# Performance work log

Hardware: AMD Instinct MI355X
Metric: run time of the kernel (lower is better)

## Reference

```python
import jax, jax.numpy as jnp
import numpy as np


def setup_inputs() -> dict:
    key = jax.random.key(0)
    k1, k2, k3, k4 = jax.random.split(key, 4)
    L, d, n_tokens = 4096, 2048, 4096
    x = jax.random.normal(k1, (L, d), dtype=jnp.float32)
    Wq_w = jax.random.normal(k2, (d, d), dtype=jnp.float32) * (1.0 / np.sqrt(d))
    Pk = jax.random.normal(k3, (1, n_tokens, d), dtype=jnp.float32)
    Pv = jax.random.normal(k4, (1, n_tokens, d), dtype=jnp.float32)
    return {"x": x, "Wq_w": Wq_w, "Pk": Pk, "Pv": Pv, "sliding_window_size": 1024}


def reference(x, Wq_w, Pk, Pv, sliding_window_size):
    # x: (L, d); Pk/Pv: (1, n_tokens, d). Single-head cross attention to a
    # fixed parameter token bank with a bidirectional sliding-window mask
    # |q_idx - kv_idx| < sliding_window_size (flex_attention semantics,
    # default scale = 1/sqrt(d)).
    L, d = x.shape
    n_tokens = Pk.shape[1]
    scale = 1.0 / np.sqrt(d).astype(np.float32)

    q = x @ Wq_w.T                                    # (L, d)
    scores = jnp.einsum('ld,td->lt', q, Pk[0]) * scale  # (L, n_tokens)

    q_idx = jnp.arange(L)[:, None]
    kv_idx = jnp.arange(n_tokens)[None, :]
    mask = jnp.abs(q_idx - kv_idx) < sliding_window_size  # (L, n_tokens)

    neg_inf = jnp.asarray(jnp.finfo(scores.dtype).min, scores.dtype)
    probs = jax.nn.softmax(jnp.where(mask, scores, neg_inf), axis=-1)
    y = jnp.einsum('lt,td->ld', probs, Pv[0])         # (L, d)
    return y[None, :, :]                              # (1, L, d) after squeeze(1)
```

## Files before the change

### kernel.cpp

```cpp
#include <hip/hip_runtime.h>


using bf16x8 = __attribute__((ext_vector_type(8))) short;
using f32x4  = __attribute__((ext_vector_type(4))) float;

#define LDIM 4096
#define TDIM 4096
#define DDIM 2048

static __device__ __forceinline__ unsigned short f2bf(float f) {
  union { float f; unsigned u; } c; c.f = f;
  unsigned r = c.u + 0x7FFFu + ((c.u >> 16) & 1u);
  return (unsigned short)(r >> 16);
}
static __device__ __forceinline__ unsigned pack2(float a, float b) {
  return (unsigned)f2bf(a) | ((unsigned)f2bf(b) << 16);
}
static __device__ __forceinline__ void gload16(const void* g, void* l) {
  __builtin_amdgcn_global_load_lds((const __attribute__((address_space(1))) void*)g,
                                   (__attribute__((address_space(3))) void*)l, 16, 0, 0);
}

__global__ __launch_bounds__(256) void k_prep(const float* __restrict__ x,
                                              const float* __restrict__ Wq,
                                              unsigned short* __restrict__ xb,
                                              unsigned short* __restrict__ wb) {
  const int tid = threadIdx.x;
  const int b = blockIdx.x;
  const float* in; unsigned short* out; size_t i;
  if (b < 4096) { in = x;  out = xb; i = (size_t)b * 256 + tid; }
  else          { in = Wq; out = wb; i = (size_t)(b - 4096) * 256 + tid; }
  const float4* p = (const float4*)(in + i * 8);
  float4 a = p[0], c = p[1];
  uint4 o = { pack2(a.x, a.y), pack2(a.z, a.w), pack2(c.x, c.y), pack2(c.z, c.w) };
  *(uint4*)(out + i * 8) = o;
}

static __device__ __forceinline__ void gemm_loop8(const unsigned short* __restrict__ A,
                                                  const unsigned short* __restrict__ B,
                                                  int m0, int n0, long lda, long ldb,
                                                  int kbeg, int kend,
                                                  unsigned short* As, unsigned short* Bs,
                                                  f32x4 (&acc)[4][2]) {
  const int tid = threadIdx.x;
  const int wave = tid >> 6, lane = tid & 63;
  const int quad = lane >> 4, l16 = lane & 15;
  const int wm = wave >> 2, wn = wave & 3;
  const int srow = wave * 16 + (lane >> 3);
  const int scb  = (lane & 7) ^ (lane >> 3);

  const unsigned short* gA = A + (long)(m0 + srow) * lda + scb * 8;
  const unsigned short* gB = B + (long)(n0 + srow) * ldb + scb * 8;
  unsigned short* lA = As + wave * 1024;
  unsigned short* lB = Bs + wave * 1024;

  const int sw = (l16 & 7) * 8;

  for (int k0 = kbeg; k0 < kend; k0 += 64) {
    gload16(gA + k0,           lA);
    gload16(gA + k0 + 8 * lda, lA + 512);
    gload16(gB + k0,           lB);
    gload16(gB + k0 + 8 * ldb, lB + 512);
    __syncthreads();
    bf16x8 af[4][2], bfr[2][2];
#pragma unroll
    for (int i = 0; i < 4; i++)
#pragma unroll
      for (int h = 0; h < 2; h++)
        af[i][h] = *(const bf16x8*)&As[(wm * 64 + i * 16 + l16) * 64 +
                                       (((h * 4 + quad) * 8) ^ sw)];
#pragma unroll
    for (int j = 0; j < 2; j++)
#pragma unroll
      for (int h = 0; h < 2; h++)
        bfr[j][h] = *(const bf16x8*)&Bs[(wn * 32 + j * 16 + l16) * 64 +
                                        (((h * 4 + quad) * 8) ^ sw)];
#pragma unroll
    for (int h = 0; h < 2; h++)
#pragma unroll
      for (int i = 0; i < 4; i++)
#pragma unroll
        for (int j = 0; j < 2; j++)
          acc[i][j] = __builtin_amdgcn_mfma_f32_16x16x32_bf16(af[i][h], bfr[j][h],
                                                              acc[i][j], 0, 0, 0);
    __syncthreads();
  }
}

__global__ __launch_bounds__(512) void k1_fused(const unsigned short* __restrict__ X,
                                                const unsigned short* __restrict__ W,
                                                const float* __restrict__ Pk,
                                                const float* __restrict__ Pv,
                                                unsigned short* __restrict__ q,
                                                unsigned short* __restrict__ kb,
                                                unsigned short* __restrict__ vt,
                                                float* __restrict__ rowsum) {
  __shared__ __align__(16) unsigned short As[128 * 64];
  __shared__ __align__(16) unsigned short Bs[128 * 64];
  const int tid = threadIdx.x;
  const int b = blockIdx.x;

  if (b < 512) {
    f32x4 acc[4][2] = {};
    const int m0 = (b >> 4) * 128, n0 = (b & 15) * 128;
    gemm_loop8(X, W, m0, n0, DDIM, DDIM, 0, DDIM, As, Bs, acc);
    const int wave = tid >> 6, lane = tid & 63;
    const int quad = lane >> 4, l16 = lane & 15, wm = wave >> 2, wn = wave & 3;
#pragma unroll
    for (int i = 0; i < 4; i++)
#pragma unroll
      for (int j = 0; j < 2; j++)
#pragma unroll
        for (int r = 0; r < 4; r++) {
          int row = m0 + wm * 64 + i * 16 + quad * 4 + r;
          int col = n0 + wn * 32 + j * 16 + l16;
          q[(long)row * DDIM + col] = f2bf(acc[i][j][r]);
        }
    return;
  }
  if (b < 2560) {
    size_t i = (size_t)(b - 512) * 512 + tid;
    const float4* p = (const float4*)(Pk + i * 8);
    float4 a = p[0], c = p[1];
    uint4 o = { pack2(a.x, a.y), pack2(a.z, a.w), pack2(c.x, c.y), pack2(c.z, c.w) };
    *(uint4*)(kb + i * 8) = o;
    return;
  }
  if (b == 4608) {
    for (int k = tid; k < LDIM; k += 512) rowsum[k] = 0.f;
    return;
  }
  unsigned short (*tile)[72] = (unsigned short (*)[72])As;
  const int b2 = b - 2560;
  const int t0 = (b2 & 63) * 64, j0 = (b2 >> 6) * 64;
  const int r = tid >> 4, c4 = (tid & 15) * 4;
#pragma unroll
  for (int rr = 0; rr < 64; rr += 32) {
    float4 v = *(const float4*)(Pv + (size_t)(t0 + r + rr) * DDIM + j0 + c4);
    tile[c4 + 0][r + rr] = f2bf(v.x);
    tile[c4 + 1][r + rr] = f2bf(v.y);
    tile[c4 + 2][r + rr] = f2bf(v.z);
    tile[c4 + 3][r + rr] = f2bf(v.w);
  }
  __syncthreads();
  const int jr = tid >> 3, tc = (tid & 7) * 8;
  *(uint4*)(vt + (size_t)(j0 + jr) * TDIM + t0 + tc) = *(const uint4*)&tile[jr][tc];
}

__global__ __launch_bounds__(512) void k2_qk(const unsigned short* __restrict__ Q,
                                             const unsigned short* __restrict__ Kb,
                                             unsigned short* __restrict__ P,
                                             float* __restrict__ rowsum,
                                             const int* __restrict__ wptr) {
  const int w = *wptr;
  const int l0 = blockIdx.y * 128, t0 = blockIdx.x * 128;
  int lo = l0 - w + 1; if (lo < 0) lo = 0;
  int hi = l0 + 127 + w - 1; if (hi > TDIM - 1) hi = TDIM - 1;
  if ((int)blockIdx.x < (lo >> 7) || (int)blockIdx.x > (hi >> 7)) return;
  __shared__ __align__(16) unsigned short As[128 * 64];
  __shared__ __align__(16) unsigned short Bs[128 * 64];
  f32x4 acc[4][2] = {};
  gemm_loop8(Q, Kb, l0, t0, DDIM, DDIM, 0, DDIM, As, Bs, acc);
  const float scale = 0.022097086912079608f;
  const int tid = threadIdx.x;
  const int wave = tid >> 6, lane = tid & 63;
  const int quad = lane >> 4, l16 = lane & 15, wm = wave >> 2, wn = wave & 3;
#pragma unroll
  for (int i = 0; i < 4; i++) {
    float rs[4] = {0.f, 0.f, 0.f, 0.f};
#pragma unroll
    for (int j = 0; j < 2; j++)
#pragma unroll
      for (int r = 0; r < 4; r++) {
        int l = l0 + wm * 64 + i * 16 + quad * 4 + r;
        int t = t0 + wn * 32 + j * 16 + l16;
        int dlt = l - t; dlt = dlt < 0 ? -dlt : dlt;
        float e = 0.f;
        if (dlt < w) e = __expf(acc[i][j][r] * scale);
        unsigned short bv = f2bf(e);
        P[(long)l * TDIM + t] = bv;
        rs[r] += __uint_as_float((unsigned)bv << 16);
      }
#pragma unroll
    for (int r = 0; r < 4; ++r) {
      float s = rs[r];
      s += __shfl_xor(s, 1);
      s += __shfl_xor(s, 2);
      s += __shfl_xor(s, 4);
      s += __shfl_xor(s, 8);
      if (l16 == 0) atomicAdd(&rowsum[l0 + wm * 64 + i * 16 + quad * 4 + r], s);
    }
  }
}

__global__ __launch_bounds__(512) void k3_pv(const unsigned short* __restrict__ P,
                                             const unsigned short* __restrict__ Vt,
                                             const float* __restrict__ rowsum,
                                             float* __restrict__ Y,
                                             const int* __restrict__ wptr) {
  const int w = *wptr;
  const int l0 = blockIdx.y * 128, j0 = blockIdx.x * 128;
  int lo = l0 - w + 1; if (lo < 0) lo = 0;
  int hi = l0 + 127 + w - 1; if (hi > TDIM - 1) hi = TDIM - 1;
  const int kb = (lo >> 7) * 128, ke = ((hi >> 7) + 1) * 128;
  __shared__ __align__(16) unsigned short As[128 * 64];
  __shared__ __align__(16) unsigned short Bs[128 * 64];
  f32x4 acc[4][2] = {};
  gemm_loop8(P, Vt, l0, j0, TDIM, TDIM, kb, ke, As, Bs, acc);
  const int tid = threadIdx.x;
  const int wave = tid >> 6, lane = tid & 63;
  const int quad = lane >> 4, l16 = lane & 15, wm = wave >> 2, wn = wave & 3;
#pragma unroll
  for (int i = 0; i < 4; i++)
#pragma unroll
    for (int r = 0; r < 4; r++) {
      const int l = l0 + wm * 64 + i * 16 + quad * 4 + r;
      const float inv = 1.0f / rowsum[l];
#pragma unroll
      for (int j = 0; j < 2; j++)
        Y[(long)l * DDIM + j0 + wn * 32 + j * 16 + l16] = acc[i][j][r] * inv;
    }
}

extern "C" void kernel_launch(void* const* d_in, const int* in_sizes, int n_in,
                              void* d_out, int out_size, void* d_ws, size_t ws_size,
                              hipStream_t stream) {
  const float* x  = (const float*)d_in[0];
  const float* Wq = (const float*)d_in[1];
  const float* Pk = (const float*)d_in[2];
  const float* Pv = (const float*)d_in[3];
  const int* wptr = (const int*)d_in[4];
  float* Y = (float*)d_out;

  unsigned short* base = (unsigned short*)d_ws;
  unsigned short* Pm = base;
  unsigned short* xb = base;
  unsigned short* wb = base + (size_t)LDIM * DDIM;
  unsigned short* kb = base + (size_t)TDIM * TDIM;
  unsigned short* vt = kb + (size_t)TDIM * DDIM;
  unsigned short* qb = vt + (size_t)DDIM * TDIM;
  float* rowsum = (float*)(qb + (size_t)LDIM * DDIM);

  k_prep<<<6144, 256, 0, stream>>>(x, Wq, xb, wb);
  k1_fused<<<4609, 512, 0, stream>>>(xb, wb, Pk, Pv, qb, kb, vt, rowsum);
  k2_qk<<<dim3(TDIM / 128, LDIM / 128), 512, 0, stream>>>(qb, kb, Pm, rowsum, wptr);
  k3_pv<<<dim3(DDIM / 128, LDIM / 128), 512, 0, stream>>>(Pm, vt, rowsum, Y, wptr);
}
```

Before: 270.7 us.

## Switch GEMMs to 1024-thread blocks with 128-wide K steps and 32x32 wave tiles

Rewrites the shared bf16 GEMM loop so each 128x128 block uses 16 waves instead of 8. Each wave computes a 32x32 sub-tile and the loop stages a 128-element K slice per iteration with a 16-way XOR swizzle. The aim is fewer barriers per K and more waves to hide latency. The cost is that each block needs twice the LDS (64KB) and each wave does fewer MFMAs per LDS fragment load. The prep/transpose branches of k1 are remapped to the new thread count, and the launch bounds now request 8 waves per EU, which may constrain register allocation.

Result: slower. 293.8 us (+8.5%).

```diff
diff --git a/kernel.cpp b/kernel.cpp
--- a/kernel.cpp
+++ b/kernel.cpp
@@ -36,143 +36,141 @@
   *(uint4*)(out + i * 8) = o;
 }
 
-static __device__ __forceinline__ void gemm_loop8(const unsigned short* __restrict__ A,
-                                                  const unsigned short* __restrict__ B,
-                                                  int m0, int n0, long lda, long ldb,
-                                                  int kbeg, int kend,
-                                                  unsigned short* As, unsigned short* Bs,
-                                                  f32x4 (&acc)[4][2]) {
+static __device__ __forceinline__ void gemm_loop16(const unsigned short* __restrict__ A,
+                                                   const unsigned short* __restrict__ B,
+                                                   int m0, int n0, long lda, long ldb,
+                                                   int kbeg, int kend,
+                                                   unsigned short* As, unsigned short* Bs,
+                                                   f32x4 (&acc)[2][2]) {
   const int tid = threadIdx.x;
   const int wave = tid >> 6, lane = tid & 63;
   const int quad = lane >> 4, l16 = lane & 15;
   const int wm = wave >> 2, wn = wave & 3;
-  const int srow = wave * 16 + (lane >> 3);
-  const int scb  = (lane & 7) ^ (lane >> 3);
-
-  const unsigned short* gA = A + (long)(m0 + srow) * lda + scb * 8;
-  const unsigned short* gB = B + (long)(n0 + srow) * ldb + scb * 8;
+  const int r0 = wave * 8 + (lane >> 4);
+  const int r1 = r0 + 4;
+  const int c  = lane & 15;
+  const int sc0 = c ^ (r0 & 15), sc1 = c ^ (r1 & 15);
+
+  const unsigned short* gA0 = A + (long)(m0 + r0) * lda + sc0 * 8;
+  const unsigned short* gA1 = A + (long)(m0 + r1) * lda + sc1 * 8;
+  const unsigned short* gB0 = B + (long)(n0 + r0) * ldb + sc0 * 8;
+  const unsigned short* gB1 = B + (long)(n0 + r1) * ldb + sc1 * 8;
   unsigned short* lA = As + wave * 1024;
   unsigned short* lB = Bs + wave * 1024;
 
-  const int sw = (l16 & 7) * 8;
-
-  for (int k0 = kbeg; k0 < kend; k0 += 64) {
-    gload16(gA + k0,           lA);
-    gload16(gA + k0 + 8 * lda, lA + 512);
-    gload16(gB + k0,           lB);
-    gload16(gB + k0 + 8 * ldb, lB + 512);
+  for (int k0 = kbeg; k0 < kend; k0 += 128) {
+    gload16(gA0 + k0, lA);
+    gload16(gA1 + k0, lA + 512);
+    gload16(gB0 + k0, lB);
+    gload16(gB1 + k0, lB + 512);
     __syncthreads();
-    bf16x8 af[4][2], bfr[2][2];
-#pragma unroll
-    for (int i = 0; i < 4; i++)
-#pragma unroll
-      for (int h = 0; h < 2; h++)
-        af[i][h] = *(const bf16x8*)&As[(wm * 64 + i * 16 + l16) * 64 +
-                                       (((h * 4 + quad) * 8) ^ sw)];
-#pragma unroll
-    for (int j = 0; j < 2; j++)
-#pragma unroll
-      for (int h = 0; h < 2; h++)
-        bfr[j][h] = *(const bf16x8*)&Bs[(wn * 32 + j * 16 + l16) * 64 +
-                                        (((h * 4 + quad) * 8) ^ sw)];
-#pragma unroll
-    for (int h = 0; h < 2; h++)
-#pragma unroll
-      for (int i = 0; i < 4; i++)
+#pragma unroll
+    for (int h = 0; h < 4; h++) {
+      bf16x8 af[2], bfr[2];
+#pragma unroll
+      for (int i = 0; i < 2; i++)
+        af[i] = *(const bf16x8*)&As[(wm * 32 + i * 16 + l16) * 128 +
+                                    (((h * 4 + quad) ^ l16) * 8)];
+#pragma unroll
+      for (int j = 0; j < 2; j++)
+        bfr[j] = *(const bf16x8*)&Bs[(wn * 32 + j * 16 + l16) * 128 +
+                                     (((h * 4 + quad) ^ l16) * 8)];
+#pragma unroll
+      for (int i = 0; i < 2; i++)
 #pragma unroll
         for (int j = 0; j < 2; j++)
-          acc[i][j] = __builtin_amdgcn_mfma_f32_16x16x32_bf16(af[i][h], bfr[j][h],
+          acc[i][j] = __builtin_amdgcn_mfma_f32_16x16x32_bf16(af[i], bfr[j],
                                                               acc[i][j], 0, 0, 0);
+    }
     __syncthreads();
   }
 }
 
-__global__ __launch_bounds__(512) void k1_fused(const unsigned short* __restrict__ X,
-                                                const unsigned short* __restrict__ W,
-                                                const float* __restrict__ Pk,
-                                                const float* __restrict__ Pv,
-                                                unsigned short* __restrict__ q,
-                                                unsigned short* __restrict__ kb,
-                                                unsigned short* __restrict__ vt,
-                                                float* __restrict__ rowsum) {
-  __shared__ __align__(16) unsigned short As[128 * 64];
-  __shared__ __align__(16) unsigned short Bs[128 * 64];
+__global__ __launch_bounds__(1024, 8) void k1_fused(const unsigned short* __restrict__ X,
+                                                    const unsigned short* __restrict__ W,
+                                                    const float* __restrict__ Pk,
+                                                    const float* __restrict__ Pv,
+                                                    unsigned short* __restrict__ q,
+                                                    unsigned short* __restrict__ kb,
+                                                    unsigned short* __restrict__ vt,
+                                                    float* __restrict__ rowsum) {
+  __shared__ __align__(16) unsigned short As[128 * 128];
+  __shared__ __align__(16) unsigned short Bs[128 * 128];
   const int tid = threadIdx.x;
   const int b = blockIdx.x;
 
   if (b < 512) {
-    f32x4 acc[4][2] = {};
+    f32x4 acc[2][2] = {};
     const int m0 = (b >> 4) * 128, n0 = (b & 15) * 128;
-    gemm_loop8(X, W, m0, n0, DDIM, DDIM, 0, DDIM, As, Bs, acc);
+    gemm_loop16(X, W, m0, n0, DDIM, DDIM, 0, DDIM, As, Bs, acc);
     const int wave = tid >> 6, lane = tid & 63;
     const int quad = lane >> 4, l16 = lane & 15, wm = wave >> 2, wn = wave & 3;
 #pragma unroll
-    for (int i = 0; i < 4; i++)
+    for (int i = 0; i < 2; i++)
 #pragma unroll
       for (int j = 0; j < 2; j++)
 #pragma unroll
         for (int r = 0; r < 4; r++) {
-          int row = m0 + wm * 64 + i * 16 + quad * 4 + r;
+          int row = m0 + wm * 32 + i * 16 + quad * 4 + r;
           int col = n0 + wn * 32 + j * 16 + l16;
           q[(long)row * DDIM + col] = f2bf(acc[i][j][r]);
         }
     return;
   }
-  if (b < 2560) {
-    size_t i = (size_t)(b - 512) * 512 + tid;
+  if (b < 1536) {
+    size_t i = (size_t)(b - 512) * 1024 + tid;
     const float4* p = (const float4*)(Pk + i * 8);
     float4 a = p[0], c = p[1];
     uint4 o = { pack2(a.x, a.y), pack2(a.z, a.w), pack2(c.x, c.y), pack2(c.z, c.w) };
     *(uint4*)(kb + i * 8) = o;
     return;
   }
-  if (b == 4608) {
-    for (int k = tid; k < LDIM; k += 512) rowsum[k] = 0.f;
+  if (b == 3584) {
+    for (int k = tid; k < LDIM; k += 1024) rowsum[k] = 0.f;
     return;
   }
   unsigned short (*tile)[72] = (unsigned short (*)[72])As;
-  const int b2 = b - 2560;
+  const int b2 = b - 1536;
   const int t0 = (b2 & 63) * 64, j0 = (b2 >> 6) * 64;
   const int r = tid >> 4, c4 = (tid & 15) * 4;
-#pragma unroll
-  for (int rr = 0; rr < 64; rr += 32) {
-    float4 v = *(const float4*)(Pv + (size_t)(t0 + r + rr) * DDIM + j0 + c4);
-    tile[c4 + 0][r + rr] = f2bf(v.x);
-    tile[c4 + 1][r + rr] = f2bf(v.y);
-    tile[c4 + 2][r + rr] = f2bf(v.z);
-    tile[c4 + 3][r + rr] = f2bf(v.w);
+  {
+    float4 v = *(const float4*)(Pv + (size_t)(t0 + r) * DDIM + j0 + c4);
+    tile[c4 + 0][r] = f2bf(v.x);
+    tile[c4 + 1][r] = f2bf(v.y);
+    tile[c4 + 2][r] = f2bf(v.z);
+    tile[c4 + 3][r] = f2bf(v.w);
   }
   __syncthreads();
-  const int jr = tid >> 3, tc = (tid & 7) * 8;
-  *(uint4*)(vt + (size_t)(j0 + jr) * TDIM + t0 + tc) = *(const uint4*)&tile[jr][tc];
-}
-
-__global__ __launch_bounds__(512) void k2_qk(const unsigned short* __restrict__ Q,
-                                             const unsigned short* __restrict__ Kb,
-                                             unsigned short* __restrict__ P,
-                                             float* __restrict__ rowsum,
-                                             const int* __restrict__ wptr) {
+  const int jr = tid >> 4, tc = (tid & 15) * 4;
+  *(uint2*)(vt + (size_t)(j0 + jr) * TDIM + t0 + tc) = *(const uint2*)&tile[jr][tc];
+}
+
+__global__ __launch_bounds__(1024, 8) void k2_qk(const unsigned short* __restrict__ Q,
+                                                 const unsigned short* __restrict__ Kb,
+                                                 unsigned short* __restrict__ P,
+                                                 float* __restrict__ rowsum,
+                                                 const int* __restrict__ wptr) {
   const int w = *wptr;
   const int l0 = blockIdx.y * 128, t0 = blockIdx.x * 128;
   int lo = l0 - w + 1; if (lo < 0) lo = 0;
   int hi = l0 + 127 + w - 1; if (hi > TDIM - 1) hi = TDIM - 1;
   if ((int)blockIdx.x < (lo >> 7) || (int)blockIdx.x > (hi >> 7)) return;
-  __shared__ __align__(16) unsigned short As[128 * 64];
-  __shared__ __align__(16) unsigned short Bs[128 * 64];
-  f32x4 acc[4][2] = {};
-  gemm_loop8(Q, Kb, l0, t0, DDIM, DDIM, 0, DDIM, As, Bs, acc);
+  __shared__ __align__(16) unsigned short As[128 * 128];
+  __shared__ __align__(16) unsigned short Bs[128 * 128];
+  f32x4 acc[2][2] = {};
+  gemm_loop16(Q, Kb, l0, t0, DDIM, DDIM, 0, DDIM, As, Bs, acc);
   const float scale = 0.022097086912079608f;
   const int tid = threadIdx.x;
   const int wave = tid >> 6, lane = tid & 63;
   const int quad = lane >> 4, l16 = lane & 15, wm = wave >> 2, wn = wave & 3;
 #pragma unroll
-  for (int i = 0; i < 4; i++) {
+  for (int i = 0; i < 2; i++) {
     float rs[4] = {0.f, 0.f, 0.f, 0.f};
 #pragma unroll
     for (int j = 0; j < 2; j++)
 #pragma unroll
       for (int r = 0; r < 4; r++) {
-        int l = l0 + wm * 64 + i * 16 + quad * 4 + r;
+        int l = l0 + wm * 32 + i * 16 + quad * 4 + r;
         int t = t0 + wn * 32 + j * 16 + l16;
         int dlt = l - t; dlt = dlt < 0 ? -dlt : dlt;
         float e = 0.f;
@@ -188,33 +186,33 @@
       s += __shfl_xor(s, 2);
       s += __shfl_xor(s, 4);
       s += __shfl_xor(s, 8);
-      if (l16 == 0) atomicAdd(&rowsum[l0 + wm * 64 + i * 16 + quad * 4 + r], s);
+      if (l16 == 0) atomicAdd(&rowsum[l0 + wm * 32 + i * 16 + quad * 4 + r], s);
     }
   }
 }
 
-__global__ __launch_bounds__(512) void k3_pv(const unsigned short* __restrict__ P,
-                                             const unsigned short* __restrict__ Vt,
-                                             const float* __restrict__ rowsum,
-                                             float* __restrict__ Y,
-                                             const int* __restrict__ wptr) {
+__global__ __launch_bounds__(1024, 8) void k3_pv(const unsigned short* __restrict__ P,
+                                                 const unsigned short* __restrict__ Vt,
+                                                 const float* __restrict__ rowsum,
+                                                 float* __restrict__ Y,
+                                                 const int* __restrict__ wptr) {
   const int w = *wptr;
   const int l0 = blockIdx.y * 128, j0 = blockIdx.x * 128;
   int lo = l0 - w + 1; if (lo < 0) lo = 0;
   int hi = l0 + 127 + w - 1; if (hi > TDIM - 1) hi = TDIM - 1;
   const int kb = (lo >> 7) * 128, ke = ((hi >> 7) + 1) * 128;
-  __shared__ __align__(16) unsigned short As[128 * 64];
-  __shared__ __align__(16) unsigned short Bs[128 * 64];
-  f32x4 acc[4][2] = {};
-  gemm_loop8(P, Vt, l0, j0, TDIM, TDIM, kb, ke, As, Bs, acc);
+  __shared__ __align__(16) unsigned short As[128 * 128];
+  __shared__ __align__(16) unsigned short Bs[128 * 128];
+  f32x4 acc[2][2] = {};
+  gemm_loop16(P, Vt, l0, j0, TDIM, TDIM, kb, ke, As, Bs, acc);
   const int tid = threadIdx.x;
   const int wave = tid >> 6, lane = tid & 63;
   const int quad = lane >> 4, l16 = lane & 15, wm = wave >> 2, wn = wave & 3;
 #pragma unroll
-  for (int i = 0; i < 4; i++)
+  for (int i = 0; i < 2; i++)
 #pragma unroll
     for (int r = 0; r < 4; r++) {
-      const int l = l0 + wm * 64 + i * 16 + quad * 4 + r;
+      const int l = l0 + wm * 32 + i * 16 + quad * 4 + r;
       const float inv = 1.0f / rowsum[l];
 #pragma unroll
       for (int j = 0; j < 2; j++)
@@ -242,7 +240,7 @@
   float* rowsum = (float*)(qb + (size_t)LDIM * DDIM);
 
   k_prep<<<6144, 256, 0, stream>>>(x, Wq, xb, wb);
-  k1_fused<<<4609, 512, 0, stream>>>(xb, wb, Pk, Pv, qb, kb, vt, rowsum);
-  k2_qk<<<dim3(TDIM / 128, LDIM / 128), 512, 0, stream>>>(qb, kb, Pm, rowsum, wptr);
-  k3_pv<<<dim3(DDIM / 128, LDIM / 128), 512, 0, stream>>>(Pm, vt, rowsum, Y, wptr);
-}
+  k1_fused<<<3585, 1024, 0, stream>>>(xb, wb, Pk, Pv, qb, kb, vt, rowsum);
+  k2_qk<<<dim3(TDIM / 128, LDIM / 128), 1024, 0, stream>>>(qb, kb, Pm, rowsum, wptr);
+  k3_pv<<<dim3(DDIM / 128, LDIM / 128), 1024, 0, stream>>>(Pm, vt, rowsum, Y, wptr);
+}
```

## Merge all stages into one persistent cooperative kernel with grid syncs

Applied to the files above, without the earlier changes.

Replaces the four separate launches (prep, Q projection plus K/V conversion, QK^T softmax numerators, PV) with one persistent cooperative kernel. Blocks loop over the tiles of each stage and meet at grid-wide barriers between stages. The aim is to remove per-launch overhead and tail gaps between kernels. In exchange it adds grid-sync costs and runs the Q GEMM and the K/V conversion one after the other instead of side by side. The aggressive launch bound (512 threads, 8 blocks) may also cap registers and cause spills. The original four-kernel path stays as a fallback if the cooperative launch fails.

Measured after the change: 848.9 us. 214% more time.

```diff
diff --git a/kernel.cpp b/kernel.cpp
--- a/kernel.cpp
+++ b/kernel.cpp
@@ -1,5 +1,8 @@
 #include <hip/hip_runtime.h>
-
+#include <hip/hip_cooperative_groups.h>
+
+
+namespace cg = cooperative_groups;
 
 using bf16x8 = __attribute__((ext_vector_type(8))) short;
 using f32x4  = __attribute__((ext_vector_type(4))) float;
@@ -19,6 +22,200 @@
 static __device__ __forceinline__ void gload16(const void* g, void* l) {
   __builtin_amdgcn_global_load_lds((const __attribute__((address_space(1))) void*)g,
                                    (__attribute__((address_space(3))) void*)l, 16, 0, 0);
+}
+
+static __device__ __forceinline__ void gemm_loop8(const unsigned short* __restrict__ A,
+                                                  const unsigned short* __restrict__ B,
+                                                  int m0, int n0, long lda, long ldb,
+                                                  int kbeg, int kend,
+                                                  unsigned short* As, unsigned short* Bs,
+                                                  f32x4 (&acc)[4][2]) {
+  const int tid = threadIdx.x;
+  const int wave = tid >> 6, lane = tid & 63;
+  const int quad = lane >> 4, l16 = lane & 15;
+  const int wm = wave >> 2, wn = wave & 3;
+  const int srow = wave * 16 + (lane >> 3);
+  const int scb  = (lane & 7) ^ (lane >> 3);
+
+  const unsigned short* gA = A + (long)(m0 + srow) * lda + scb * 8;
+  const unsigned short* gB = B + (long)(n0 + srow) * ldb + scb * 8;
+  unsigned short* lA = As + wave * 1024;
+  unsigned short* lB = Bs + wave * 1024;
+
+  const int sw = (l16 & 7) * 8;
+
+  for (int k0 = kbeg; k0 < kend; k0 += 64) {
+    gload16(gA + k0,           lA);
+    gload16(gA + k0 + 8 * lda, lA + 512);
+    gload16(gB + k0,           lB);
+    gload16(gB + k0 + 8 * ldb, lB + 512);
+    __syncthreads();
+    bf16x8 af[4][2], bfr[2][2];
+#pragma unroll
+    for (int i = 0; i < 4; i++)
+#pragma unroll
+      for (int h = 0; h < 2; h++)
+        af[i][h] = *(const bf16x8*)&As[(wm * 64 + i * 16 + l16) * 64 +
+                                       (((h * 4 + quad) * 8) ^ sw)];
+#pragma unroll
+    for (int j = 0; j < 2; j++)
+#pragma unroll
+      for (int h = 0; h < 2; h++)
+        bfr[j][h] = *(const bf16x8*)&Bs[(wn * 32 + j * 16 + l16) * 64 +
+                                        (((h * 4 + quad) * 8) ^ sw)];
+#pragma unroll
+    for (int h = 0; h < 2; h++)
+#pragma unroll
+      for (int i = 0; i < 4; i++)
+#pragma unroll
+        for (int j = 0; j < 2; j++)
+          acc[i][j] = __builtin_amdgcn_mfma_f32_16x16x32_bf16(af[i][h], bfr[j][h],
+                                                              acc[i][j], 0, 0, 0);
+    __syncthreads();
+  }
+}
+
+__global__ __launch_bounds__(512, 8) void mega(const float* __restrict__ x,
+                                               const float* __restrict__ Wq,
+                                               const float* __restrict__ Pk,
+                                               const float* __restrict__ Pv,
+                                               const int* __restrict__ wptr,
+                                               unsigned short* __restrict__ xb,
+                                               unsigned short* __restrict__ wb,
+                                               unsigned short* __restrict__ kb,
+                                               unsigned short* __restrict__ vt,
+                                               unsigned short* __restrict__ qb,
+                                               unsigned short* __restrict__ Pm,
+                                               float* __restrict__ rowsum,
+                                               float* __restrict__ Y) {
+  __shared__ __align__(16) unsigned short As[128 * 64];
+  __shared__ __align__(16) unsigned short Bs[128 * 64];
+  const int tid = threadIdx.x;
+  const int bid = blockIdx.x;
+  const int G = gridDim.x;
+  cg::grid_group grid = cg::this_grid();
+
+  const int wave = tid >> 6, lane = tid & 63;
+  const int quad = lane >> 4, l16 = lane & 15;
+  const int wm = wave >> 2, wn = wave & 3;
+
+  for (int t = bid; t < 3072; t += G) {
+    const float* in; unsigned short* out; size_t i;
+    if (t < 2048) { in = x;  out = xb; i = (size_t)t * 512 + tid; }
+    else          { in = Wq; out = wb; i = (size_t)(t - 2048) * 512 + tid; }
+    const float4* p = (const float4*)(in + i * 8);
+    float4 a = p[0], c = p[1];
+    uint4 o = { pack2(a.x, a.y), pack2(a.z, a.w), pack2(c.x, c.y), pack2(c.z, c.w) };
+    *(uint4*)(out + i * 8) = o;
+  }
+  __threadfence();
+  grid.sync();
+
+  for (int t = bid; t < 512; t += G) {
+    f32x4 acc[4][2] = {};
+    const int m0 = (t >> 4) * 128, n0 = (t & 15) * 128;
+    gemm_loop8(xb, wb, m0, n0, DDIM, DDIM, 0, DDIM, As, Bs, acc);
+#pragma unroll
+    for (int i = 0; i < 4; i++)
+#pragma unroll
+      for (int j = 0; j < 2; j++)
+#pragma unroll
+        for (int r = 0; r < 4; r++) {
+          int row = m0 + wm * 64 + i * 16 + quad * 4 + r;
+          int col = n0 + wn * 32 + j * 16 + l16;
+          qb[(long)row * DDIM + col] = f2bf(acc[i][j][r]);
+        }
+  }
+  for (int t = bid; t < 4097; t += G) {
+    if (t < 2048) {
+      size_t i = (size_t)t * 512 + tid;
+      const float4* p = (const float4*)(Pk + i * 8);
+      float4 a = p[0], c = p[1];
+      uint4 o = { pack2(a.x, a.y), pack2(a.z, a.w), pack2(c.x, c.y), pack2(c.z, c.w) };
+      *(uint4*)(kb + i * 8) = o;
+    } else if (t < 4096) {
+      unsigned short (*tile)[72] = (unsigned short (*)[72])As;
+      const int u = t - 2048;
+      const int t0 = (u & 63) * 64, j0 = (u >> 6) * 64;
+      const int r = tid >> 4, c4 = (tid & 15) * 4;
+      __syncthreads();
+#pragma unroll
+      for (int rr = 0; rr < 64; rr += 32) {
+        float4 v = *(const float4*)(Pv + (size_t)(t0 + r + rr) * DDIM + j0 + c4);
+        tile[c4 + 0][r + rr] = f2bf(v.x);
+        tile[c4 + 1][r + rr] = f2bf(v.y);
+        tile[c4 + 2][r + rr] = f2bf(v.z);
+        tile[c4 + 3][r + rr] = f2bf(v.w);
+      }
+      __syncthreads();
+      const int jr = tid >> 3, tc = (tid & 7) * 8;
+      *(uint4*)(vt + (size_t)(j0 + jr) * TDIM + t0 + tc) = *(const uint4*)&tile[jr][tc];
+    } else {
+      for (int k = tid; k < LDIM; k += 512) rowsum[k] = 0.f;
+    }
+  }
+  __threadfence();
+  grid.sync();
+
+  const int w = *wptr;
+  const float scale = 0.022097086912079608f;
+  for (int t = bid; t < 1024; t += G) {
+    const int bx = t & 31, by = t >> 5;
+    const int l0 = by * 128, t0 = bx * 128;
+    int lo = l0 - w + 1; if (lo < 0) lo = 0;
+    int hi = l0 + 127 + w - 1; if (hi > TDIM - 1) hi = TDIM - 1;
+    if (bx < (lo >> 7) || bx > (hi >> 7)) continue;
+    f32x4 acc[4][2] = {};
+    gemm_loop8(qb, kb, l0, t0, DDIM, DDIM, 0, DDIM, As, Bs, acc);
+#pragma unroll
+    for (int i = 0; i < 4; i++) {
+      float rs[4] = {0.f, 0.f, 0.f, 0.f};
+#pragma unroll
+      for (int j = 0; j < 2; j++)
+#pragma unroll
+        for (int r = 0; r < 4; r++) {
+          int l = l0 + wm * 64 + i * 16 + quad * 4 + r;
+          int tt = t0 + wn * 32 + j * 16 + l16;
+          int dlt = l - tt; dlt = dlt < 0 ? -dlt : dlt;
+          float e = 0.f;
+          if (dlt < w) e = __expf(acc[i][j][r] * scale);
+          unsigned short bv = f2bf(e);
+          Pm[(long)l * TDIM + tt] = bv;
+          rs[r] += __uint_as_float((unsigned)bv << 16);
+        }
+#pragma unroll
+      for (int r = 0; r < 4; ++r) {
+        float s = rs[r];
+        s += __shfl_xor(s, 1);
+        s += __shfl_xor(s, 2);
+        s += __shfl_xor(s, 4);
+        s += __shfl_xor(s, 8);
+        if (l16 == 0) atomicAdd(&rowsum[l0 + wm * 64 + i * 16 + quad * 4 + r], s);
+      }
+    }
+  }
+  __threadfence();
+  grid.sync();
+
+  for (int t = bid; t < 512; t += G) {
+    const int bx = t & 15, by = t >> 4;
+    const int l0 = by * 128, j0 = bx * 128;
+    int lo = l0 - w + 1; if (lo < 0) lo = 0;
+    int hi = l0 + 127 + w - 1; if (hi > TDIM - 1) hi = TDIM - 1;
+    const int kb2 = (lo >> 7) * 128, ke = ((hi >> 7) + 1) * 128;
+    f32x4 acc[4][2] = {};
+    gemm_loop8(Pm, vt, l0, j0, TDIM, TDIM, kb2, ke, As, Bs, acc);
+#pragma unroll
+    for (int i = 0; i < 4; i++)
+#pragma unroll
+      for (int r = 0; r < 4; r++) {
+        const int l = l0 + wm * 64 + i * 16 + quad * 4 + r;
+        const float inv = 1.0f / rowsum[l];
+#pragma unroll
+        for (int j = 0; j < 2; j++)
+          Y[(long)l * DDIM + j0 + wn * 32 + j * 16 + l16] = acc[i][j][r] * inv;
+      }
+  }
 }
 
 __global__ __launch_bounds__(256) void k_prep(const float* __restrict__ x,
@@ -34,57 +231,6 @@
   float4 a = p[0], c = p[1];
   uint4 o = { pack2(a.x, a.y), pack2(a.z, a.w), pack2(c.x, c.y), pack2(c.z, c.w) };
   *(uint4*)(out + i * 8) = o;
-}
-
-static __device__ __forceinline__ void gemm_loop8(const unsigned short* __restrict__ A,
-                                                  const unsigned short* __restrict__ B,
-                                                  int m0, int n0, long lda, long ldb,
-                                                  int kbeg, int kend,
-                                                  unsigned short* As, unsigned short* Bs,
-                                                  f32x4 (&acc)[4][2]) {
-  const int tid = threadIdx.x;
-  const int wave = tid >> 6, lane = tid & 63;
-  const int quad = lane >> 4, l16 = lane & 15;
-  const int wm = wave >> 2, wn = wave & 3;
-  const int srow = wave * 16 + (lane >> 3);
-  const int scb  = (lane & 7) ^ (lane >> 3);
-
-  const unsigned short* gA = A + (long)(m0 + srow) * lda + scb * 8;
-  const unsigned short* gB = B + (long)(n0 + srow) * ldb + scb * 8;
-  unsigned short* lA = As + wave * 1024;
-  unsigned short* lB = Bs + wave * 1024;
-
-  const int sw = (l16 & 7) * 8;
-
-  for (int k0 = kbeg; k0 < kend; k0 += 64) {
-    gload16(gA + k0,           lA);
-    gload16(gA + k0 + 8 * lda, lA + 512);
-    gload16(gB + k0,           lB);
-    gload16(gB + k0 + 8 * ldb, lB + 512);
-    __syncthreads();
-    bf16x8 af[4][2], bfr[2][2];
-#pragma unroll
-    for (int i = 0; i < 4; i++)
-#pragma unroll
-      for (int h = 0; h < 2; h++)
-        af[i][h] = *(const bf16x8*)&As[(wm * 64 + i * 16 + l16) * 64 +
-                                       (((h * 4 + quad) * 8) ^ sw)];
-#pragma unroll
-    for (int j = 0; j < 2; j++)
-#pragma unroll
-      for (int h = 0; h < 2; h++)
-        bfr[j][h] = *(const bf16x8*)&Bs[(wn * 32 + j * 16 + l16) * 64 +
-                                        (((h * 4 + quad) * 8) ^ sw)];
-#pragma unroll
-    for (int h = 0; h < 2; h++)
-#pragma unroll
-      for (int i = 0; i < 4; i++)
-#pragma unroll
-        for (int j = 0; j < 2; j++)
-          acc[i][j] = __builtin_amdgcn_mfma_f32_16x16x32_bf16(af[i][h], bfr[j][h],
-                                                              acc[i][j], 0, 0, 0);
-    __syncthreads();
-  }
 }
 
 __global__ __launch_bounds__(512) void k1_fused(const unsigned short* __restrict__ X,
@@ -99,7 +245,6 @@
   __shared__ __align__(16) unsigned short Bs[128 * 64];
   const int tid = threadIdx.x;
   const int b = blockIdx.x;
-
   if (b < 512) {
     f32x4 acc[4][2] = {};
     const int m0 = (b >> 4) * 128, n0 = (b & 15) * 128;
@@ -122,7 +267,8 @@
     size_t i = (size_t)(b - 512) * 512 + tid;
     const float4* p = (const float4*)(Pk + i * 8);
     float4 a = p[0], c = p[1];
-    uint4 o = { pack2(a.x, a.y), pack2(a.z, a.w), pack2(c.x, c.y), pack2(c.z, c.w) };
+    uint4 o = { pack2(a.x, a.y), pack2(a.z, a.w), pack2(c.x, c.y), pack2(c.w, c.w) };
+    o.w = pack2(c.z, c.w);
     *(uint4*)(kb + i * 8) = o;
     return;
   }
@@ -241,8 +387,25 @@
   unsigned short* qb = vt + (size_t)DDIM * TDIM;
   float* rowsum = (float*)(qb + (size_t)LDIM * DDIM);
 
-  k_prep<<<6144, 256, 0, stream>>>(x, Wq, xb, wb);
-  k1_fused<<<4609, 512, 0, stream>>>(xb, wb, Pk, Pv, qb, kb, vt, rowsum);
-  k2_qk<<<dim3(TDIM / 128, LDIM / 128), 512, 0, stream>>>(qb, kb, Pm, rowsum, wptr);
-  k3_pv<<<dim3(DDIM / 128, LDIM / 128), 512, 0, stream>>>(Pm, vt, rowsum, Y, wptr);
-}
+  static int gblocks = -1;
+  if (gblocks < 0) {
+    int per_cu = 0;
+    if (hipOccupancyMaxActiveBlocksPerMultiprocessor(&per_cu, mega, 512, 0) != hipSuccess ||
+        per_cu <= 0)
+      per_cu = 2;
+    gblocks = per_cu * 256;
+    if (gblocks > 1024) gblocks = 1024;
+  }
+
+  void* args[] = { (void*)&x, (void*)&Wq, (void*)&Pk, (void*)&Pv, (void*)&wptr,
+                   (void*)&xb, (void*)&wb, (void*)&kb, (void*)&vt, (void*)&qb,
+                   (void*)&Pm, (void*)&rowsum, (void*)&Y };
+  hipError_t err = hipLaunchCooperativeKernel((const void*)mega, dim3(gblocks),
+                                              dim3(512), args, 0, stream);
+  if (err != hipSuccess) {
+    k_prep<<<6144, 256, 0, stream>>>(x, Wq, xb, wb);
+    k1_fused<<<4609, 512, 0, stream>>>(xb, wb, Pk, Pv, qb, kb, vt, rowsum);
+    k2_qk<<<dim3(TDIM / 128, LDIM / 128), 512, 0, stream>>>(qb, kb, Pm, rowsum, wptr);
+    k3_pv<<<dim3(DDIM / 128, LDIM / 128), 512, 0, stream>>>(Pm, vt, rowsum, Y, wptr);
+  }
+}
```
